# Optimization experiments

Measured on AMD Instinct MI355X. Metric: run time of the kernel, lower is better.

The kernel has to match this reference:

```python
import jax, jax.numpy as jnp
import numpy as np

EPS = 0.05        # entropic regularization
TEMP = 0.1        # softmax temperature
ITERS = 3         # min sinkhorn iterations
TOL = 1e-3        # convergence tolerance
MAX_ITERS = 100   # max sinkhorn iterations
TINY = 1e-12

B, K, C = 4096, 3000, 8


def _sinkhorn(scores):
    """Balanced assignments Q[B,K]: rows sum ~1, cols sum ~B/K. Detached."""
    Bn, Kn = scores.shape
    S = scores.astype(jnp.float32) / EPS
    S = S - jnp.max(S, axis=1, keepdims=True)
    Q = jnp.exp(S)
    target_c = jnp.float32(Bn / Kn)

    def cond(state):
        _, _, _, done = state
        return jnp.logical_not(done)

    def body(state):
        u, v, it, _ = state
        u = 1.0 / (Q @ v.T + TINY)              # [B,1], a = ones
        v = target_c / (u.T @ Q + TINY)          # [1,K], b = B/K * ones
        it = it + 1
        P = u * Q * v
        row_err = jnp.max(jnp.abs(jnp.sum(P, axis=1) - 1.0))
        col_err = jnp.max(jnp.abs(jnp.sum(P, axis=0) - target_c))
        err = jnp.maximum(row_err, col_err)
        done = (it >= ITERS) & ((it >= MAX_ITERS) | (err <= TOL))
        return (u, v, it, done)

    u0 = jnp.ones((Bn, 1), jnp.float32)
    v0 = jnp.ones((1, Kn), jnp.float32)
    u, v, _, _ = jax.lax.while_loop(cond, body, (u0, v0, jnp.int32(0), jnp.bool_(False)))
    P = u * Q * v
    P = P / jnp.clip(jnp.sum(P, axis=1, keepdims=True), TINY, None)
    P = P * (target_c / jnp.clip(jnp.sum(P, axis=0, keepdims=True), TINY, None))
    P = P / jnp.clip(jnp.sum(P, axis=1, keepdims=True), TINY, None)
    return jax.lax.stop_gradient(P)


def setup_inputs() -> dict:
    key = jax.random.key(0)
    keys = jax.random.split(key, C)
    inp = {f"logits{c}": jax.random.normal(keys[c], (B, K), dtype=jnp.float32)
           for c in range(C)}
    inp["idx_a"] = 0
    inp["idx_b"] = 1
    return inp


def reference(logits0, logits1, logits2, logits3, logits4, logits5, logits6, logits7, idx_a, idx_b):
    crops = [logits0, logits1, logits2, logits3, logits4, logits5, logits6, logits7]
    Qa = _sinkhorn(crops[idx_a])
    Qb = _sinkhorn(crops[idx_b])

    def entropy(Q):
        return -jnp.mean(jnp.sum(Q * jnp.log(Q + TINY), axis=1))

    ent = 0.5 * (entropy(Qa) + entropy(Qb))
    q_max_mean = 0.5 * (jnp.mean(jnp.max(Qa, axis=1)) + jnp.mean(jnp.max(Qb, axis=1)))

    losses = []
    for c, lg in enumerate(crops):
        logp = jax.nn.log_softmax(lg.astype(jnp.float32) / TEMP, axis=1)
        if c != idx_a:
            losses.append(-jnp.mean(jnp.sum(Qa * logp, axis=1)))
        if c != idx_b:
            losses.append(-jnp.mean(jnp.sum(Qb * logp, axis=1)))
    loss = jnp.mean(jnp.stack(losses))
    return (loss, ent, q_max_mean)
```

## Files before the change

### kernel.cpp

```cpp
#include <hip/hip_runtime.h>
#include <hip/hip_cooperative_groups.h>
#include <math.h>

namespace cg = cooperative_groups;

struct Ptr8 { const float* p[8]; };

#define Bn 4096
#define Kn 3000
#define KQ4 750
#define KP 3072
#define INV_EPS 20.0f
#define INV_TEMP 10.0f
#define TINYF 1e-12f
#define TOLF 1e-3f
#define TGTC (4096.0f/3000.0f)

#define CAPR 448
#define CAPC 448
#define CUTF 1.4f

#define BLD_NBLK 2048

#define IT_NBLK 64
#define IT_THR 1024
#define IT_NWAVE (IT_NBLK * IT_THR / 64)
#define MAXC 6
#define MAXR 8
#define BARSTRIDE 32

#define ALD(p)    __hip_atomic_load((p), __ATOMIC_RELAXED, __HIP_MEMORY_SCOPE_AGENT)
#define AST(p, x) __hip_atomic_store((p), (x), __ATOMIC_RELAXED, __HIP_MEMORY_SCOPE_AGENT)

#define NSTR 12
#define NCH 40
#define GRID_S 480
#define NW_S (GRID_S * 4)

__device__ __forceinline__ float wsum(float x) {
#pragma unroll
  for (int o = 32; o; o >>= 1) x += __shfl_xor(x, o, 64);
  return x;
}
__device__ __forceinline__ float wmax(float x) {
#pragma unroll
  for (int o = 32; o; o >>= 1) x = fmaxf(x, __shfl_xor(x, o, 64));
  return x;
}
__device__ __forceinline__ float block_max(float x) {
  __shared__ float s[4];
  x = wmax(x);
  if ((threadIdx.x & 63) == 0) s[threadIdx.x >> 6] = x;
  __syncthreads();
  float r = fmaxf(fmaxf(s[0], s[1]), fmaxf(s[2], s[3]));
  __syncthreads();
  return r;
}

struct BuildArgs {
  Ptr8 ptrs;
  const int* iap; const int* ibp;
  float* pmA; float* pmB;
  float* r;
  unsigned* rowcnt;
  unsigned* colcnt;
  float* csrq; unsigned short* csridx;
  float* cscq; unsigned short* cscidx;
};

__global__ __launch_bounds__(256, 2) void build_sparse(BuildArgs a) {
  const int tid = threadIdx.x;
  const int lane = tid & 63;
  const int wv = blockIdx.x * 4 + (tid >> 6);
  const int crop = wv >> 12;
  const int row = wv & (Bn - 1);
  const int idx = ((crop ? *a.ibp : *a.iap) & 7);
  const float* __restrict__ lg = a.ptrs.p[idx];
  const float4* rp = (const float4*)(lg + (size_t)row * Kn);

  float M = -INFINITY, T = 0.f;
  for (int i = lane; i < KQ4; i += 64) {
    float4 x = rp[i];
    float m4 = fmaxf(fmaxf(x.x, x.y), fmaxf(x.z, x.w));
    float t4 = __expf((x.x - m4) * INV_EPS) + __expf((x.y - m4) * INV_EPS)
             + __expf((x.z - m4) * INV_EPS) + __expf((x.w - m4) * INV_EPS);
    float Mn = fmaxf(M, m4);
    T = T * __expf((M - Mn) * INV_EPS) + t4 * __expf((m4 - Mn) * INV_EPS);
    M = Mn;
  }
#pragma unroll
  for (int o = 32; o; o >>= 1) {
    float M2 = __shfl_xor(M, o, 64);
    float T2 = __shfl_xor(T, o, 64);
    float Mn = fmaxf(M, M2);
    T = T * __expf((M - Mn) * INV_EPS) + T2 * __expf((M2 - Mn) * INV_EPS);
    M = Mn;
  }
  if (lane == 0) {
    (crop ? a.pmB : a.pmA)[row] = M;
    a.r[crop * Bn + row] = T;
  }
  const float thr = M - CUTF;

  int cnt = 0;
  for (int i = lane; i < KQ4; i += 64) {
    float4 x = rp[i];
    cnt += (x.x >= thr) + (x.y >= thr) + (x.z >= thr) + (x.w >= thr);
  }
  int incl = cnt;
#pragma unroll
  for (int o = 1; o < 64; o <<= 1) {
    int t = __shfl_up(incl, o, 64);
    if (lane >= o) incl += t;
  }
  int total = __shfl(incl, 63, 64);
  int p = incl - cnt;
  if (lane == 0) a.rowcnt[crop * Bn + row] = (unsigned)min(total, CAPR);

  float* crow = a.csrq + ((size_t)crop * Bn + row) * CAPR;
  unsigned short* cidx = a.csridx + ((size_t)crop * Bn + row) * CAPR;
  unsigned* ccnt = a.colcnt + crop * KP;
  float* cq_ = a.cscq + (size_t)crop * KP * CAPC;
  unsigned short* ci_ = a.cscidx + (size_t)crop * KP * CAPC;

  for (int i = lane; i < KQ4; i += 64) {
    float4 x = rp[i];
    int k0 = i * 4;
#define EMIT(val, kk)                                                          \
    if ((val) >= thr) {                                                        \
      float q = __expf(((val) - M) * INV_EPS);                                 \
      if (p < CAPR) { crow[p] = q; cidx[p] = (unsigned short)(kk); }           \
      unsigned slot = atomicAdd(&ccnt[kk], 1u);                                \
      if (slot < CAPC) {                                                       \
        size_t o2 = (size_t)(kk) * CAPC + slot;                                \
        cq_[o2] = q; ci_[o2] = (unsigned short)row;                            \
      }                                                                        \
      ++p;                                                                     \
    }
    EMIT(x.x, k0 + 0) EMIT(x.y, k0 + 1) EMIT(x.z, k0 + 2) EMIT(x.w, k0 + 3)
#undef EMIT
  }
}

struct ItArgs {
  float* pAa; float* pCa; float* pAb; float* pCb;
  float* u; float* r; float* v;
  const unsigned* rowcnt; const unsigned* colcnt;
  const float* csrq; const unsigned short* csridx;
  const float* cscq; const unsigned short* cscidx;
  unsigned* err;
  unsigned* arrive;
  unsigned* release;
};

__device__ __forceinline__ void gbar2(unsigned* arrive, unsigned* release, unsigned g) {
  __syncthreads();
  if (threadIdx.x == 0)
    AST(&arrive[blockIdx.x * BARSTRIDE], g);
  if (blockIdx.x == 0) {
    if (threadIdx.x < 64) {
      while ((int)(ALD(&arrive[threadIdx.x * BARSTRIDE]) - g) < 0)
        __builtin_amdgcn_s_sleep(1);
    }
    __syncthreads();
    if (threadIdx.x == 0) AST(release, g);
  } else {
    if (threadIdx.x == 0) {
      while ((int)(ALD(release) - g) < 0)
        __builtin_amdgcn_s_sleep(1);
    }
  }
  __syncthreads();
}

__global__ __launch_bounds__(IT_THR) void sinkhorn_iterate(ItArgs a) {
  const int tid = threadIdx.x;
  const int lane = tid & 63;
  const int bid = blockIdx.x;
  const int wv = bid * (IT_THR / 64) + (tid >> 6);

  __shared__ float lds_rinv[2 * Bn];
  __shared__ float lds_v[2 * KP];
  __shared__ float2 sred[16];
  __shared__ float serr[2];

  int cN[MAXC], cCrop[MAXC];
#pragma unroll
  for (int s = 0; s < MAXC; ++s) {
    int vc = wv + s * IT_NWAVE;
    if (vc < 2 * Kn) {
      int crop = vc >= Kn;
      cCrop[s] = crop;
      cN[s] = min((int)a.colcnt[crop * KP + (vc - crop * Kn)], CAPC);
    } else { cCrop[s] = -1; cN[s] = 0; }
  }
  int rN[MAXR];
#pragma unroll
  for (int s = 0; s < MAXR; ++s) {
    int vr = wv + s * IT_NWAVE;
    rN[s] = min((int)a.rowcnt[vr], CAPR);
  }

  unsigned gen = 0;
  bool done0 = false, done1 = false;
  int it = 0;
  while (true) {
    ++it;
    const int par = it & 1;
    for (int g = tid; g < 2 * Bn; g += IT_THR) {
      int cr = g >> 12;
      if (!(cr ? done1 : done0))
        lds_rinv[g] = 1.0f / (ALD(&a.r[g]) + TINYF);
    }
    __syncthreads();
    float cerr0 = 0.f, cerr1 = 0.f;
#pragma unroll
    for (int s = 0; s < MAXC; ++s) {
      int cc = cCrop[s];
      if (cc < 0) continue;
      if (cc ? done1 : done0) continue;
      int vc = wv + s * IT_NWAVE;
      int col = vc - cc * Kn;
      size_t base = ((size_t)cc * KP + col) * CAPC;
      const float* q = a.cscq + base;
      const unsigned short* ix = a.cscidx + base;
      int n = cN[s];
      float acc = 0.f;
      for (int j = lane; j < n; j += 64) acc += q[j] * lds_rinv[cc * Bn + ix[j]];
      acc = wsum(acc);
      float vk = TGTC / (acc + TINYF);
      if (lane == 0) AST(&a.v[cc * KP + col], vk);
      float e = fabsf(vk * acc - TGTC);
      if (cc) cerr1 = fmaxf(cerr1, e); else cerr0 = fmaxf(cerr0, e);
    }
    if (it >= 3) {
      cerr0 = wmax(cerr0); cerr1 = wmax(cerr1);
      if (lane == 0) sred[tid >> 6] = make_float2(cerr0, cerr1);
      __syncthreads();
      if (tid == 0) {
        float m0 = sred[0].x, m1 = sred[0].y;
#pragma unroll
        for (int i = 1; i < 16; ++i) { m0 = fmaxf(m0, sred[i].x); m1 = fmaxf(m1, sred[i].y); }
        if (!done0) AST(&a.err[par * 256 + 64 + bid], __float_as_uint(m0));
        if (!done1) AST(&a.err[par * 256 + 192 + bid], __float_as_uint(m1));
      }
    }
    gbar2(a.arrive, a.release, ++gen);
    for (int g = tid; g < 2 * KP; g += IT_THR) {
      int cr = g >= KP;
      if (!(cr ? done1 : done0))
        lds_v[g] = ALD(&a.v[g]);
    }
    __syncthreads();
    float lerr0 = 0.f, lerr1 = 0.f;
#pragma unroll
    for (int s = 0; s < MAXR; ++s) {
      int vr = wv + s * IT_NWAVE;
      int crop = vr >= Bn;
      if (crop ? done1 : done0) continue;
      size_t base = (size_t)vr * CAPR;
      const float* q = a.csrq + base;
      const unsigned short* ix = a.csridx + base;
      int n = rN[s];
      float acc = 0.f;
      for (int j = lane; j < n; j += 64) acc += q[j] * lds_v[crop * KP + ix[j]];
      acc = wsum(acc);
      float uu = lds_rinv[vr];
      if (lane == 0) {
        AST(&a.u[vr], uu);
        AST(&a.r[vr], acc);
      }
      float e = fabsf(uu * acc - 1.0f);
      if (crop) lerr1 = fmaxf(lerr1, e); else lerr0 = fmaxf(lerr0, e);
    }
    if (it >= 3) {
      lerr0 = wmax(lerr0); lerr1 = wmax(lerr1);
      if (lane == 0) sred[tid >> 6] = make_float2(lerr0, lerr1);
      __syncthreads();
      if (tid == 0) {
        float m0 = sred[0].x, m1 = sred[0].y;
#pragma unroll
        for (int i = 1; i < 16; ++i) { m0 = fmaxf(m0, sred[i].x); m1 = fmaxf(m1, sred[i].y); }
        if (!done0) AST(&a.err[par * 256 + bid], __float_as_uint(m0));
        if (!done1) AST(&a.err[par * 256 + 128 + bid], __float_as_uint(m1));
      }
    }
    gbar2(a.arrive, a.release, ++gen);
    if (it >= 3) {
      if (tid < 64) {
        float e0 = __uint_as_float(ALD(&a.err[par * 256 + tid]));
        float e1 = __uint_as_float(ALD(&a.err[par * 256 + 64 + tid]));
        float e2 = __uint_as_float(ALD(&a.err[par * 256 + 128 + tid]));
        float e3 = __uint_as_float(ALD(&a.err[par * 256 + 192 + tid]));
        float eA = wmax(fmaxf(e0, e1));
        float eB = wmax(fmaxf(e2, e3));
        if (tid == 0) { serr[0] = eA; serr[1] = eB; }
      }
      __syncthreads();
      if (!done0) done0 = (it >= 100) || (serr[0] <= TOLF);
      if (!done1) done1 = (it >= 100) || (serr[1] <= TOLF);
      __syncthreads();
      if (done0 && done1) break;
    }
  }

  for (int g = tid; g < 2 * Bn; g += IT_THR) {
    float uu = ALD(&a.u[g]);
    float rr = ALD(&a.r[g]);
    lds_rinv[g] = uu / fmaxf(uu * rr, TINYF);
  }
  __syncthreads();
#pragma unroll
  for (int s = 0; s < MAXC; ++s) {
    int cc = cCrop[s];
    if (cc < 0) continue;
    int vc = wv + s * IT_NWAVE;
    int col = vc - cc * Kn;
    size_t base = ((size_t)cc * KP + col) * CAPC;
    const float* q = a.cscq + base;
    const unsigned short* ix = a.cscidx + base;
    int n = cN[s];
    float d = 0.f;
    for (int j = lane; j < n; j += 64) d += q[j] * lds_rinv[cc * Bn + ix[j]];
    d = wsum(d);
    float vk = lds_v[cc * KP + col];
    if (lane == 0)
      AST(&(cc ? a.pCb : a.pCa)[col], vk * TGTC / fmaxf(vk * d, TINYF));
  }
  gbar2(a.arrive, a.release, ++gen);
  for (int g = tid; g < 2 * KP; g += IT_THR) {
    int cr = g >= KP;
    lds_v[g] = ALD(&(cr ? a.pCb : a.pCa)[g - cr * KP]);
  }
  __syncthreads();
#pragma unroll
  for (int s = 0; s < MAXR; ++s) {
    int vr = wv + s * IT_NWAVE;
    int crop = vr >= Bn;
    size_t base = (size_t)vr * CAPR;
    const float* q = a.csrq + base;
    const unsigned short* ix = a.csridx + base;
    int n = rN[s];
    float e = 0.f;
    for (int j = lane; j < n; j += 64) e += q[j] * lds_v[crop * KP + ix[j]];
    e = wsum(e);
    if (lane == 0) {
      float al = lds_rinv[vr];
      (crop ? a.pAb : a.pAa)[vr - crop * Bn] = al / fmaxf(al * e, TINYF);
    }
  }
}

__global__ __launch_bounds__(256, 2) void sinkhorn_dense(
    Ptr8 ptrs, const int* __restrict__ idxp,
    float* __restrict__ ws_m, float* __restrict__ ws_u, float* __restrict__ ws_r,
    float* __restrict__ ws_A, float* __restrict__ ws_v, float* __restrict__ ws_C,
    float* __restrict__ cpart, unsigned* __restrict__ errbuf)
{
  cg::grid_group grid = cg::this_grid();
  const int idx = (*idxp) & 7;
  const float* __restrict__ lg = ptrs.p[idx];
  const int tid = threadIdx.x;
  const int lane = tid & 63;
  const int gw = blockIdx.x * 4 + (tid >> 6);
  const int stripe = blockIdx.x % NSTR;
  const int chunk = blockIdx.x / NSTR;
  const int kcol = stripe * 256 + tid;
  const int rs = (chunk * Bn) / NCH;
  const int re = ((chunk + 1) * Bn) / NCH;

  for (int row = gw; row < Bn; row += NW_S) {
    const float4* rp = (const float4*)(lg + (size_t)row * Kn);
    float M = -INFINITY, T = 0.f;
    for (int i = lane; i < KQ4; i += 64) {
      float4 x = rp[i];
      float m4 = fmaxf(fmaxf(x.x, x.y), fmaxf(x.z, x.w));
      float t4 = __expf((x.x - m4) * INV_EPS) + __expf((x.y - m4) * INV_EPS)
               + __expf((x.z - m4) * INV_EPS) + __expf((x.w - m4) * INV_EPS);
      float Mn = fmaxf(M, m4);
      T = T * __expf((M - Mn) * INV_EPS) + t4 * __expf((m4 - Mn) * INV_EPS);
      M = Mn;
    }
#pragma unroll
    for (int o = 32; o; o >>= 1) {
      float M2 = __shfl_xor(M, o, 64);
      float T2 = __shfl_xor(T, o, 64);
      float Mn = fmaxf(M, M2);
      T = T * __expf((M - Mn) * INV_EPS) + T2 * __expf((M2 - Mn) * INV_EPS);
      M = Mn;
    }
    if (lane == 0) { ws_m[row] = M; ws_r[row] = T; }
  }
  grid.sync(); __threadfence();

  int it = 0;
  while (true) {
    ++it;
    {
      float acc = 0.f;
      if (kcol < Kn) {
        for (int row = rs; row < re; ++row) {
          float u = 1.0f / (ws_r[row] + TINYF);
          acc += u * __expf((lg[(size_t)row * Kn + kcol] - ws_m[row]) * INV_EPS);
        }
      }
      cpart[chunk * KP + stripe * 256 + tid] = acc;
    }
    grid.sync(); __threadfence();
    {
      int k = blockIdx.x * 256 + tid;
      float cerr = 0.f;
      if (k < Kn) {
        float c = 0.f;
        for (int ch = 0; ch < NCH; ++ch) c += cpart[ch * KP + k];
        float vk = TGTC / (c + TINYF);
        ws_v[k] = vk;
        cerr = fabsf(vk * c - TGTC);
      }
      float bm = block_max(cerr);
      if (tid == 0) atomicMax(&errbuf[2 * it + 1], __float_as_uint(bm));
    }
    grid.sync(); __threadfence();
    {
      float lerr = 0.f;
      for (int row = gw; row < Bn; row += NW_S) {
        const float4* rp = (const float4*)(lg + (size_t)row * Kn);
        const float4* vp = (const float4*)ws_v;
        float mm = ws_m[row];
        float u = 1.0f / (ws_r[row] + TINYF);
        float Ssum = 0.f;
        for (int i = lane; i < KQ4; i += 64) {
          float4 x = rp[i];
          float4 vv = vp[i];
          Ssum += __expf((x.x - mm) * INV_EPS) * vv.x
                + __expf((x.y - mm) * INV_EPS) * vv.y
                + __expf((x.z - mm) * INV_EPS) * vv.z
                + __expf((x.w - mm) * INV_EPS) * vv.w;
        }
        Ssum = wsum(Ssum);
        if (lane == 0) { ws_u[row] = u; ws_r[row] = Ssum; }
        lerr = fmaxf(lerr, fabsf(u * Ssum - 1.0f));
      }
      float bm = block_max(lerr);
      if (tid == 0) atomicMax(&errbuf[2 * it], __float_as_uint(bm));
    }
    grid.sync(); __threadfence();
    unsigned rbits = __hip_atomic_load(&errbuf[2 * it], __ATOMIC_RELAXED, __HIP_MEMORY_SCOPE_AGENT);
    unsigned cbits = __hip_atomic_load(&errbuf[2 * it + 1], __ATOMIC_RELAXED, __HIP_MEMORY_SCOPE_AGENT);
    float err = fmaxf(__uint_as_float(rbits), __uint_as_float(cbits));
    if (it >= 3 && (it >= 100 || err <= TOLF)) break;
  }

  {
    float acc = 0.f;
    if (kcol < Kn) {
      for (int row = rs; row < re; ++row) {
        float u = ws_u[row];
        float sp = fmaxf(u * ws_r[row], TINYF);
        acc += (u / sp) * __expf((lg[(size_t)row * Kn + kcol] - ws_m[row]) * INV_EPS);
      }
    }
    cpart[chunk * KP + stripe * 256 + tid] = acc;
  }
  grid.sync(); __threadfence();
  {
    int k = blockIdx.x * 256 + tid;
    if (k < Kn) {
      float d = 0.f;
      for (int ch = 0; ch < NCH; ++ch) d += cpart[ch * KP + k];
      float vk = ws_v[k];
      ws_C[k] = vk * TGTC / fmaxf(vk * d, TINYF);
    }
  }
  grid.sync(); __threadfence();
  {
    for (int row = gw; row < Bn; row += NW_S) {
      const float4* rp = (const float4*)(lg + (size_t)row * Kn);
      const float4* cp = (const float4*)ws_C;
      float mm = ws_m[row];
      float e = 0.f;
      for (int i = lane; i < KQ4; i += 64) {
        float4 x = rp[i];
        float4 cc = cp[i];
        e += __expf((x.x - mm) * INV_EPS) * cc.x
           + __expf((x.y - mm) * INV_EPS) * cc.y
           + __expf((x.z - mm) * INV_EPS) * cc.z
           + __expf((x.w - mm) * INV_EPS) * cc.w;
      }
      e = wsum(e);
      if (lane == 0) {
        float u = ws_u[row];
        float sp = fmaxf(u * ws_r[row], TINYF);
        float us = u / sp;
        float w = us * e;
        ws_A[row] = us / fmaxf(w, TINYF);
      }
    }
  }
}

__global__ __launch_bounds__(256) void loss_kernel(
    Ptr8 ptrs, const int* __restrict__ iap, const int* __restrict__ ibp,
    const float* __restrict__ wsa, const float* __restrict__ wsb,
    float* __restrict__ out)
{
  const int ia = (*iap) & 7;
  const int ib = (*ibp) & 7;
  const int lane = threadIdx.x & 63;
  const int row = blockIdx.x * 4 + (threadIdx.x >> 6);

  const float ma = wsa[row];
  const float Aa = wsa[4096 + row];
  const float mb = wsb[row];
  const float Ab = wsb[4096 + row];
  const float4* Ca4 = (const float4*)(wsa + 8192);
  const float4* Cb4 = (const float4*)(wsb + 8192);
  size_t off = (size_t)row * Kn;
  const float4* X4[8];
#pragma unroll
  for (int c = 0; c < 8; ++c) X4[c] = (const float4*)(ptrs.p[c] + off);
  const float4* xa4 = (const float4*)(ptrs.p[ia] + off);
  const float4* xb4 = (const float4*)(ptrs.p[ib] + off);

  float M[8], S[8], da[8], db[8];
#pragma unroll
  for (int c = 0; c < 8; ++c) { M[c] = -INFINITY; S[c] = 0.f; da[c] = 0.f; db[c] = 0.f; }
  float enta = 0.f, entb = 0.f, ra = 0.f, rb = 0.f, qam = 0.f, qbm = 0.f;

  for (int i = lane; i < KQ4; i += 64) {
    float4 xa = xa4[i], xb = xb4[i];
    float4 ca = Ca4[i], cb = Cb4[i];
    float qa0 = __expf((xa.x - ma) * INV_EPS) * Aa * ca.x;
    float qa1 = __expf((xa.y - ma) * INV_EPS) * Aa * ca.y;
    float qa2 = __expf((xa.z - ma) * INV_EPS) * Aa * ca.z;
    float qa3 = __expf((xa.w - ma) * INV_EPS) * Aa * ca.w;
    float qb0 = __expf((xb.x - mb) * INV_EPS) * Ab * cb.x;
    float qb1 = __expf((xb.y - mb) * INV_EPS) * Ab * cb.y;
    float qb2 = __expf((xb.z - mb) * INV_EPS) * Ab * cb.z;
    float qb3 = __expf((xb.w - mb) * INV_EPS) * Ab * cb.w;
    ra += (qa0 + qa1) + (qa2 + qa3);
    rb += (qb0 + qb1) + (qb2 + qb3);
    enta += qa0 * __logf(qa0 + TINYF) + qa1 * __logf(qa1 + TINYF)
          + qa2 * __logf(qa2 + TINYF) + qa3 * __logf(qa3 + TINYF);
    entb += qb0 * __logf(qb0 + TINYF) + qb1 * __logf(qb1 + TINYF)
          + qb2 * __logf(qb2 + TINYF) + qb3 * __logf(qb3 + TINYF);
    qam = fmaxf(qam, fmaxf(fmaxf(qa0, qa1), fmaxf(qa2, qa3)));
    qbm = fmaxf(qbm, fmaxf(fmaxf(qb0, qb1), fmaxf(qb2, qb3)));
#pragma unroll
    for (int c = 0; c < 8; ++c) {
      float4 x = X4[c][i];
      float y0 = x.x * INV_TEMP, y1 = x.y * INV_TEMP;
      float y2 = x.z * INV_TEMP, y3 = x.w * INV_TEMP;
      float m4 = fmaxf(fmaxf(y0, y1), fmaxf(y2, y3));
      float t4 = __expf(y0 - m4) + __expf(y1 - m4) + __expf(y2 - m4) + __expf(y3 - m4);
      float Mn = fmaxf(M[c], m4);
      S[c] = S[c] * __expf(M[c] - Mn) + t4 * __expf(m4 - Mn);
      M[c] = Mn;
      da[c] += qa0 * x.x + qa1 * x.y + qa2 * x.z + qa3 * x.w;
      db[c] += qb0 * x.x + qb1 * x.y + qb2 * x.z + qb3 * x.w;
    }
  }

#pragma unroll
  for (int c = 0; c < 8; ++c) {
#pragma unroll
    for (int o = 32; o; o >>= 1) {
      float M2 = __shfl_xor(M[c], o, 64);
      float S2 = __shfl_xor(S[c], o, 64);
      float Mn = fmaxf(M[c], M2);
      S[c] = S[c] * __expf(M[c] - Mn) + S2 * __expf(M2 - Mn);
      M[c] = Mn;
    }
    da[c] = wsum(da[c]);
    db[c] = wsum(db[c]);
  }
  enta = wsum(enta); entb = wsum(entb);
  ra = wsum(ra); rb = wsum(rb);
  qam = wmax(qam); qbm = wmax(qbm);

  if (lane == 0) {
    float lsum = 0.f;
    int nt = 0;
#pragma unroll
    for (int c = 0; c < 8; ++c) {
      float L = M[c] + __logf(S[c]);
      if (c != ia) { lsum -= INV_TEMP * da[c] - L * ra; ++nt; }
      if (c != ib) { lsum -= INV_TEMP * db[c] - L * rb; ++nt; }
    }
    atomicAdd(&out[0], lsum / ((float)nt * (float)Bn));
    atomicAdd(&out[1], -0.5f / (float)Bn * (enta + entb));
    atomicAdd(&out[2], 0.5f / (float)Bn * (qam + qbm));
  }
}

extern "C" void kernel_launch(void* const* d_in, const int* in_sizes, int n_in,
                              void* d_out, int out_size, void* d_ws, size_t ws_size,
                              hipStream_t stream)
{
  (void)in_sizes; (void)n_in; (void)out_size;
  Ptr8 ptrs;
  for (int c = 0; c < 8; ++c) ptrs.p[c] = (const float*)d_in[c];
  const int* iap = (const int*)d_in[8];
  const int* ibp = (const int*)d_in[9];
  float* ws = (float*)d_ws;
  float* out = (float*)d_out;

  float* PA = ws;
  float* PB = ws + 11264;
  float* u_ = ws + 22528;
  float* r_ = ws + 30720;
  float* v_ = ws + 38912;
  unsigned* rowcnt = (unsigned*)(ws + 45056);
  unsigned* colcnt = (unsigned*)(ws + 53248);
  unsigned* err = (unsigned*)(ws + 59392);
  unsigned* arrive = (unsigned*)(ws + 59904);
  unsigned* release = (unsigned*)(ws + 61952);
  float* csrq = ws + 62016;
  unsigned short* csridx = (unsigned short*)(ws + 3732032);
  float* cscq = ws + 5567040;
  unsigned short* cscidx = (unsigned short*)(ws + 8319552);
  const size_t need_bytes = (size_t)9695808 * 4;

  hipMemsetAsync(colcnt, 0, 8768 * sizeof(unsigned), stream);
  hipMemsetAsync(d_out, 0, 3 * sizeof(float), stream);

  if (ws_size >= need_bytes) {
    BuildArgs ba;
    ba.ptrs = ptrs; ba.iap = iap; ba.ibp = ibp;
    ba.pmA = PA; ba.pmB = PB;
    ba.r = r_;
    ba.rowcnt = rowcnt; ba.colcnt = colcnt;
    ba.csrq = csrq; ba.csridx = csridx; ba.cscq = cscq; ba.cscidx = cscidx;
    hipLaunchKernelGGL(build_sparse, dim3(BLD_NBLK), dim3(256), 0, stream, ba);

    ItArgs ia;
    ia.pAa = PA + 4096; ia.pCa = PA + 8192;
    ia.pAb = PB + 4096; ia.pCb = PB + 8192;
    ia.u = u_; ia.r = r_; ia.v = v_;
    ia.rowcnt = rowcnt; ia.colcnt = colcnt;
    ia.csrq = csrq; ia.csridx = csridx; ia.cscq = cscq; ia.cscidx = cscidx;
    ia.err = err; ia.arrive = arrive; ia.release = release;
    void* args1[] = { (void*)&ia };
    hipLaunchCooperativeKernel((const void*)sinkhorn_iterate, dim3(IT_NBLK), dim3(IT_THR),
                               (void**)args1, 0u, stream);
  } else {
    float* cpart = ws + 62016;
    unsigned* errA = err;
    unsigned* errB = err + 256;
    {
      float* m = PA; float* A = PA + 4096; float* C = PA + 8192;
      void* args[] = { (void*)&ptrs, (void*)&iap, (void*)&m, (void*)&u_, (void*)&r_,
                       (void*)&A, (void*)&v_, (void*)&C, (void*)&cpart, (void*)&errA };
      hipLaunchCooperativeKernel((const void*)sinkhorn_dense, dim3(GRID_S), dim3(256),
                                 (void**)args, 0u, stream);
    }
    {
      float* m = PB; float* A = PB + 4096; float* C = PB + 8192;
      void* args[] = { (void*)&ptrs, (void*)&ibp, (void*)&m, (void*)&u_, (void*)&r_,
                       (void*)&A, (void*)&v_, (void*)&C, (void*)&cpart, (void*)&errB };
      hipLaunchCooperativeKernel((const void*)sinkhorn_dense, dim3(GRID_S), dim3(256),
                                 (void**)args, 0u, stream);
    }
  }

  loss_kernel<<<dim3(Bn / 4), dim3(256), 0, stream>>>(ptrs, iap, ibp, PA, PB, out);
}
```

Before: 3.788 ms.

## Shrink Sinkhorn iterate grid and fuse error reduction into the grid barrier

The persistent iteration kernel drops from 64 to 16 blocks, so each wave handles more rows and columns. The error reduction now travels inside the barrier: each block packs its generation and error into a 64-bit arrive word, and block 0 folds the convergence decision into the release flag. That removes the separate error buffer and the extra read phase after each barrier. Reciprocal row sums are precomputed and stored in place of the u vector, and per-wave counts are reloaded each iteration instead of being cached in registers. Fewer blocks make barriers cheaper but leave less parallelism for the sparse gathers.

```diff
diff --git a/kernel.cpp b/kernel.cpp
--- a/kernel.cpp
+++ b/kernel.cpp
@@ -22,12 +22,12 @@
 
 #define BLD_NBLK 2048
 
-#define IT_NBLK 64
+#define IT_NBLK 16
 #define IT_THR 1024
-#define IT_NWAVE (IT_NBLK * IT_THR / 64)
-#define MAXC 6
-#define MAXR 8
-#define BARSTRIDE 32
+#define IT_NW (IT_NBLK * IT_THR / 64)
+#define MAXC ((2*Kn + IT_NW - 1) / IT_NW)
+#define MAXR ((2*Bn) / IT_NW)
+#define ABAR_STRIDE 16
 
 #define ALD(p)    __hip_atomic_load((p), __ATOMIC_RELAXED, __HIP_MEMORY_SCOPE_AGENT)
 #define AST(p, x) __hip_atomic_store((p), (x), __ATOMIC_RELAXED, __HIP_MEMORY_SCOPE_AGENT)
@@ -61,7 +61,7 @@
   Ptr8 ptrs;
   const int* iap; const int* ibp;
   float* pmA; float* pmB;
-  float* r;
+  float* r; float* rinv;
   unsigned* rowcnt;
   unsigned* colcnt;
   float* csrq; unsigned short* csridx;
@@ -99,6 +99,7 @@
   if (lane == 0) {
     (crop ? a.pmB : a.pmA)[row] = M;
     a.r[crop * Bn + row] = T;
+    a.rinv[crop * Bn + row] = 1.0f / (T + TINYF);
   }
   const float thr = M - CUTF;
 
@@ -144,34 +145,13 @@
 
 struct ItArgs {
   float* pAa; float* pCa; float* pAb; float* pCb;
-  float* u; float* r; float* v;
+  float* r; float* rinv; float* v;
   const unsigned* rowcnt; const unsigned* colcnt;
   const float* csrq; const unsigned short* csridx;
   const float* cscq; const unsigned short* cscidx;
-  unsigned* err;
-  unsigned* arrive;
+  unsigned long long* arrive;
   unsigned* release;
 };
-
-__device__ __forceinline__ void gbar2(unsigned* arrive, unsigned* release, unsigned g) {
-  __syncthreads();
-  if (threadIdx.x == 0)
-    AST(&arrive[blockIdx.x * BARSTRIDE], g);
-  if (blockIdx.x == 0) {
-    if (threadIdx.x < 64) {
-      while ((int)(ALD(&arrive[threadIdx.x * BARSTRIDE]) - g) < 0)
-        __builtin_amdgcn_s_sleep(1);
-    }
-    __syncthreads();
-    if (threadIdx.x == 0) AST(release, g);
-  } else {
-    if (threadIdx.x == 0) {
-      while ((int)(ALD(release) - g) < 0)
-        __builtin_amdgcn_s_sleep(1);
-    }
-  }
-  __syncthreads();
-}
 
 __global__ __launch_bounds__(IT_THR) void sinkhorn_iterate(ItArgs a) {
   const int tid = threadIdx.x;
@@ -181,50 +161,32 @@
 
   __shared__ float lds_rinv[2 * Bn];
   __shared__ float lds_v[2 * KP];
-  __shared__ float2 sred[16];
-  __shared__ float serr[2];
-
-  int cN[MAXC], cCrop[MAXC];
-#pragma unroll
-  for (int s = 0; s < MAXC; ++s) {
-    int vc = wv + s * IT_NWAVE;
-    if (vc < 2 * Kn) {
-      int crop = vc >= Kn;
-      cCrop[s] = crop;
-      cN[s] = min((int)a.colcnt[crop * KP + (vc - crop * Kn)], CAPC);
-    } else { cCrop[s] = -1; cN[s] = 0; }
-  }
-  int rN[MAXR];
-#pragma unroll
-  for (int s = 0; s < MAXR; ++s) {
-    int vr = wv + s * IT_NWAVE;
-    rN[s] = min((int)a.rowcnt[vr], CAPR);
-  }
+  __shared__ float sredA[16], sredB[16];
+  __shared__ float scerr[2];
+  __shared__ unsigned sflag;
 
   unsigned gen = 0;
   bool done0 = false, done1 = false;
   int it = 0;
   while (true) {
     ++it;
-    const int par = it & 1;
     for (int g = tid; g < 2 * Bn; g += IT_THR) {
       int cr = g >> 12;
-      if (!(cr ? done1 : done0))
-        lds_rinv[g] = 1.0f / (ALD(&a.r[g]) + TINYF);
+      if (!(cr ? done1 : done0)) lds_rinv[g] = ALD(&a.rinv[g]);
     }
     __syncthreads();
     float cerr0 = 0.f, cerr1 = 0.f;
-#pragma unroll
+#pragma unroll 4
     for (int s = 0; s < MAXC; ++s) {
-      int cc = cCrop[s];
-      if (cc < 0) continue;
+      int vc = wv + s * IT_NW;
+      if (vc >= 2 * Kn) break;
+      int cc = vc >= Kn;
       if (cc ? done1 : done0) continue;
-      int vc = wv + s * IT_NWAVE;
       int col = vc - cc * Kn;
       size_t base = ((size_t)cc * KP + col) * CAPC;
       const float* q = a.cscq + base;
       const unsigned short* ix = a.cscidx + base;
-      int n = cN[s];
+      int n = min((int)a.colcnt[cc * KP + col], CAPC);
       float acc = 0.f;
       for (int j = lane; j < n; j += 64) acc += q[j] * lds_rinv[cc * Bn + ix[j]];
       acc = wsum(acc);
@@ -233,93 +195,139 @@
       float e = fabsf(vk * acc - TGTC);
       if (cc) cerr1 = fmaxf(cerr1, e); else cerr0 = fmaxf(cerr0, e);
     }
-    if (it >= 3) {
-      cerr0 = wmax(cerr0); cerr1 = wmax(cerr1);
-      if (lane == 0) sred[tid >> 6] = make_float2(cerr0, cerr1);
-      __syncthreads();
+    cerr0 = wmax(cerr0); cerr1 = wmax(cerr1);
+    if (lane == 0) { sredA[tid >> 6] = cerr0; sredB[tid >> 6] = cerr1; }
+    __syncthreads();
+    ++gen;
+    if (tid == 0) {
+      float m0 = sredA[0], m1 = sredB[0];
+#pragma unroll
+      for (int i = 1; i < 16; ++i) { m0 = fmaxf(m0, sredA[i]); m1 = fmaxf(m1, sredB[i]); }
+      AST(&a.arrive[bid * ABAR_STRIDE],     ((unsigned long long)gen << 32) | __float_as_uint(m0));
+      AST(&a.arrive[bid * ABAR_STRIDE + 1], ((unsigned long long)gen << 32) | __float_as_uint(m1));
+    }
+    if (bid == 0) {
+      if (tid < 64) {
+        float errv = 0.f;
+        if (lane < 2 * IT_NBLK) {
+          unsigned long long w;
+          for (;;) {
+            w = ALD(&a.arrive[(lane >> 1) * ABAR_STRIDE + (lane & 1)]);
+            if ((int)((unsigned)(w >> 32) - gen) >= 0) break;
+            __builtin_amdgcn_s_sleep(1);
+          }
+          errv = __uint_as_float((unsigned)w);
+        }
+        if (tid == 0)
+          AST(a.release, (gen << 2) | (done0 ? 2u : 0u) | (done1 ? 1u : 0u));
+        float eA = wmax(((lane & 1) == 0) ? errv : 0.f);
+        float eB = wmax(((lane & 1) == 1) ? errv : 0.f);
+        if (tid == 0) { scerr[0] = eA; scerr[1] = eB; }
+      }
+    } else {
       if (tid == 0) {
-        float m0 = sred[0].x, m1 = sred[0].y;
-#pragma unroll
-        for (int i = 1; i < 16; ++i) { m0 = fmaxf(m0, sred[i].x); m1 = fmaxf(m1, sred[i].y); }
-        if (!done0) AST(&a.err[par * 256 + 64 + bid], __float_as_uint(m0));
-        if (!done1) AST(&a.err[par * 256 + 192 + bid], __float_as_uint(m1));
-      }
-    }
-    gbar2(a.arrive, a.release, ++gen);
+        for (;;) {
+          unsigned rv = ALD(a.release);
+          if ((int)((rv >> 2) - gen) >= 0) break;
+          __builtin_amdgcn_s_sleep(1);
+        }
+      }
+    }
+    __syncthreads();
     for (int g = tid; g < 2 * KP; g += IT_THR) {
       int cr = g >= KP;
-      if (!(cr ? done1 : done0))
-        lds_v[g] = ALD(&a.v[g]);
+      if (!(cr ? done1 : done0)) lds_v[g] = ALD(&a.v[g]);
     }
     __syncthreads();
     float lerr0 = 0.f, lerr1 = 0.f;
-#pragma unroll
+#pragma unroll 4
     for (int s = 0; s < MAXR; ++s) {
-      int vr = wv + s * IT_NWAVE;
+      int vr = wv + s * IT_NW;
       int crop = vr >= Bn;
       if (crop ? done1 : done0) continue;
       size_t base = (size_t)vr * CAPR;
       const float* q = a.csrq + base;
       const unsigned short* ix = a.csridx + base;
-      int n = rN[s];
+      int n = min((int)a.rowcnt[vr], CAPR);
       float acc = 0.f;
       for (int j = lane; j < n; j += 64) acc += q[j] * lds_v[crop * KP + ix[j]];
       acc = wsum(acc);
       float uu = lds_rinv[vr];
       if (lane == 0) {
-        AST(&a.u[vr], uu);
         AST(&a.r[vr], acc);
+        AST(&a.rinv[vr], 1.0f / (acc + TINYF));
       }
       float e = fabsf(uu * acc - 1.0f);
       if (crop) lerr1 = fmaxf(lerr1, e); else lerr0 = fmaxf(lerr0, e);
     }
-    if (it >= 3) {
-      lerr0 = wmax(lerr0); lerr1 = wmax(lerr1);
-      if (lane == 0) sred[tid >> 6] = make_float2(lerr0, lerr1);
-      __syncthreads();
+    lerr0 = wmax(lerr0); lerr1 = wmax(lerr1);
+    if (lane == 0) { sredA[tid >> 6] = lerr0; sredB[tid >> 6] = lerr1; }
+    __syncthreads();
+    ++gen;
+    if (tid == 0) {
+      float m0 = sredA[0], m1 = sredB[0];
+#pragma unroll
+      for (int i = 1; i < 16; ++i) { m0 = fmaxf(m0, sredA[i]); m1 = fmaxf(m1, sredB[i]); }
+      AST(&a.arrive[bid * ABAR_STRIDE],     ((unsigned long long)gen << 32) | __float_as_uint(m0));
+      AST(&a.arrive[bid * ABAR_STRIDE + 1], ((unsigned long long)gen << 32) | __float_as_uint(m1));
+    }
+    if (bid == 0) {
+      if (tid < 64) {
+        float errv = 0.f;
+        if (lane < 2 * IT_NBLK) {
+          unsigned long long w;
+          for (;;) {
+            w = ALD(&a.arrive[(lane >> 1) * ABAR_STRIDE + (lane & 1)]);
+            if ((int)((unsigned)(w >> 32) - gen) >= 0) break;
+            __builtin_amdgcn_s_sleep(1);
+          }
+          errv = __uint_as_float((unsigned)w);
+        }
+        float eA = wmax(((lane & 1) == 0) ? errv : 0.f);
+        float eB = wmax(((lane & 1) == 1) ? errv : 0.f);
+        if (tid == 0) {
+          float errA = fmaxf(scerr[0], eA);
+          float errB = fmaxf(scerr[1], eB);
+          bool d0 = done0 || ((it >= 3) && (it >= 100 || errA <= TOLF));
+          bool d1 = done1 || ((it >= 3) && (it >= 100 || errB <= TOLF));
+          unsigned rel = (gen << 2) | (d0 ? 2u : 0u) | (d1 ? 1u : 0u);
+          sflag = rel;
+          AST(a.release, rel);
+        }
+      }
+    } else {
       if (tid == 0) {
-        float m0 = sred[0].x, m1 = sred[0].y;
-#pragma unroll
-        for (int i = 1; i < 16; ++i) { m0 = fmaxf(m0, sred[i].x); m1 = fmaxf(m1, sred[i].y); }
-        if (!done0) AST(&a.err[par * 256 + bid], __float_as_uint(m0));
-        if (!done1) AST(&a.err[par * 256 + 128 + bid], __float_as_uint(m1));
-      }
-    }
-    gbar2(a.arrive, a.release, ++gen);
-    if (it >= 3) {
-      if (tid < 64) {
-        float e0 = __uint_as_float(ALD(&a.err[par * 256 + tid]));
-        float e1 = __uint_as_float(ALD(&a.err[par * 256 + 64 + tid]));
-        float e2 = __uint_as_float(ALD(&a.err[par * 256 + 128 + tid]));
-        float e3 = __uint_as_float(ALD(&a.err[par * 256 + 192 + tid]));
-        float eA = wmax(fmaxf(e0, e1));
-        float eB = wmax(fmaxf(e2, e3));
-        if (tid == 0) { serr[0] = eA; serr[1] = eB; }
-      }
-      __syncthreads();
-      if (!done0) done0 = (it >= 100) || (serr[0] <= TOLF);
-      if (!done1) done1 = (it >= 100) || (serr[1] <= TOLF);
-      __syncthreads();
-      if (done0 && done1) break;
-    }
+        unsigned rv;
+        for (;;) {
+          rv = ALD(a.release);
+          if ((int)((rv >> 2) - gen) >= 0) break;
+          __builtin_amdgcn_s_sleep(1);
+        }
+        sflag = rv;
+      }
+    }
+    __syncthreads();
+    done0 = (sflag >> 1) & 1;
+    done1 = sflag & 1;
+    if (done0 && done1) break;
   }
 
   for (int g = tid; g < 2 * Bn; g += IT_THR) {
-    float uu = ALD(&a.u[g]);
+    float uu = lds_rinv[g];
     float rr = ALD(&a.r[g]);
     lds_rinv[g] = uu / fmaxf(uu * rr, TINYF);
   }
   __syncthreads();
-#pragma unroll
+#pragma unroll 4
   for (int s = 0; s < MAXC; ++s) {
-    int cc = cCrop[s];
-    if (cc < 0) continue;
-    int vc = wv + s * IT_NWAVE;
+    int vc = wv + s * IT_NW;
+    if (vc >= 2 * Kn) break;
+    int cc = vc >= Kn;
     int col = vc - cc * Kn;
     size_t base = ((size_t)cc * KP + col) * CAPC;
     const float* q = a.cscq + base;
     const unsigned short* ix = a.cscidx + base;
-    int n = cN[s];
+    int n = min((int)a.colcnt[cc * KP + col], CAPC);
     float d = 0.f;
     for (int j = lane; j < n; j += 64) d += q[j] * lds_rinv[cc * Bn + ix[j]];
     d = wsum(d);
@@ -327,20 +335,45 @@
     if (lane == 0)
       AST(&(cc ? a.pCb : a.pCa)[col], vk * TGTC / fmaxf(vk * d, TINYF));
   }
-  gbar2(a.arrive, a.release, ++gen);
+  __syncthreads();
+  ++gen;
+  if (tid == 0) {
+    AST(&a.arrive[bid * ABAR_STRIDE], ((unsigned long long)gen << 32));
+  }
+  if (bid == 0) {
+    if (tid < 64) {
+      if (lane < IT_NBLK) {
+        for (;;) {
+          unsigned long long w = ALD(&a.arrive[lane * ABAR_STRIDE]);
+          if ((int)((unsigned)(w >> 32) - gen) >= 0) break;
+          __builtin_amdgcn_s_sleep(1);
+        }
+      }
+      if (tid == 0) AST(a.release, (gen << 2) | 3u);
+    }
+  } else {
+    if (tid == 0) {
+      for (;;) {
+        unsigned rv = ALD(a.release);
+        if ((int)((rv >> 2) - gen) >= 0) break;
+        __builtin_amdgcn_s_sleep(1);
+      }
+    }
+  }
+  __syncthreads();
   for (int g = tid; g < 2 * KP; g += IT_THR) {
     int cr = g >= KP;
     lds_v[g] = ALD(&(cr ? a.pCb : a.pCa)[g - cr * KP]);
   }
   __syncthreads();
-#pragma unroll
+#pragma unroll 4
   for (int s = 0; s < MAXR; ++s) {
-    int vr = wv + s * IT_NWAVE;
+    int vr = wv + s * IT_NW;
     int crop = vr >= Bn;
     size_t base = (size_t)vr * CAPR;
     const float* q = a.csrq + base;
     const unsigned short* ix = a.csridx + base;
-    int n = rN[s];
+    int n = min((int)a.rowcnt[vr], CAPR);
     float e = 0.f;
     for (int j = lane; j < n; j += 64) e += q[j] * lds_v[crop * KP + ix[j]];
     e = wsum(e);
@@ -607,28 +640,27 @@
 
   float* PA = ws;
   float* PB = ws + 11264;
-  float* u_ = ws + 22528;
-  float* r_ = ws + 30720;
+  float* r_ = ws + 22528;
+  float* ri_ = ws + 30720;
   float* v_ = ws + 38912;
   unsigned* rowcnt = (unsigned*)(ws + 45056);
   unsigned* colcnt = (unsigned*)(ws + 53248);
-  unsigned* err = (unsigned*)(ws + 59392);
-  unsigned* arrive = (unsigned*)(ws + 59904);
-  unsigned* release = (unsigned*)(ws + 61952);
-  float* csrq = ws + 62016;
-  unsigned short* csridx = (unsigned short*)(ws + 3732032);
-  float* cscq = ws + 5567040;
-  unsigned short* cscidx = (unsigned short*)(ws + 8319552);
-  const size_t need_bytes = (size_t)9695808 * 4;
-
-  hipMemsetAsync(colcnt, 0, 8768 * sizeof(unsigned), stream);
+  unsigned long long* arrive = (unsigned long long*)(ws + 59392);
+  unsigned* release = (unsigned*)(ws + 59904);
+  float* csrq = ws + 59968;
+  unsigned short* csridx = (unsigned short*)(ws + 3729984);
+  float* cscq = ws + 5564992;
+  unsigned short* cscidx = (unsigned short*)(ws + 8317504);
+  const size_t need_bytes = (size_t)9693760 * 4;
+
+  hipMemsetAsync(colcnt, 0, 6720 * sizeof(unsigned), stream);
   hipMemsetAsync(d_out, 0, 3 * sizeof(float), stream);
 
   if (ws_size >= need_bytes) {
     BuildArgs ba;
     ba.ptrs = ptrs; ba.iap = iap; ba.ibp = ibp;
     ba.pmA = PA; ba.pmB = PB;
-    ba.r = r_;
+    ba.r = r_; ba.rinv = ri_;
     ba.rowcnt = rowcnt; ba.colcnt = colcnt;
     ba.csrq = csrq; ba.csridx = csridx; ba.cscq = cscq; ba.cscidx = cscidx;
     hipLaunchKernelGGL(build_sparse, dim3(BLD_NBLK), dim3(256), 0, stream, ba);
@@ -636,27 +668,27 @@
     ItArgs ia;
     ia.pAa = PA + 4096; ia.pCa = PA + 8192;
     ia.pAb = PB + 4096; ia.pCb = PB + 8192;
-    ia.u = u_; ia.r = r_; ia.v = v_;
+    ia.r = r_; ia.rinv = ri_; ia.v = v_;
     ia.rowcnt = rowcnt; ia.colcnt = colcnt;
     ia.csrq = csrq; ia.csridx = csridx; ia.cscq = cscq; ia.cscidx = cscidx;
-    ia.err = err; ia.arrive = arrive; ia.release = release;
+    ia.arrive = arrive; ia.release = release;
     void* args1[] = { (void*)&ia };
     hipLaunchCooperativeKernel((const void*)sinkhorn_iterate, dim3(IT_NBLK), dim3(IT_THR),
                                (void**)args1, 0u, stream);
   } else {
-    float* cpart = ws + 62016;
-    unsigned* errA = err;
-    unsigned* errB = err + 256;
+    float* cpart = ws + 59968;
+    unsigned* errA = colcnt;
+    unsigned* errB = colcnt + 256;
     {
       float* m = PA; float* A = PA + 4096; float* C = PA + 8192;
-      void* args[] = { (void*)&ptrs, (void*)&iap, (void*)&m, (void*)&u_, (void*)&r_,
+      void* args[] = { (void*)&ptrs, (void*)&iap, (void*)&m, (void*)&ri_, (void*)&r_,
                        (void*)&A, (void*)&v_, (void*)&C, (void*)&cpart, (void*)&errA };
       hipLaunchCooperativeKernel((const void*)sinkhorn_dense, dim3(GRID_S), dim3(256),
                                  (void**)args, 0u, stream);
     }
     {
       float* m = PB; float* A = PB + 4096; float* C = PB + 8192;
-      void* args[] = { (void*)&ptrs, (void*)&ibp, (void*)&m, (void*)&u_, (void*)&r_,
+      void* args[] = { (void*)&ptrs, (void*)&ibp, (void*)&m, (void*)&ri_, (void*)&r_,
                        (void*)&A, (void*)&v_, (void*)&C, (void*)&cpart, (void*)&errB };
       hipLaunchCooperativeKernel((const void*)sinkhorn_dense, dim3(GRID_S), dim3(256),
                                  (void**)args, 0u, stream);
```

After: 7.687 ms. 2.03x slower.
